# Kernel tuning notes

Measured on AMD Instinct MI355X. Metric: run time of the kernel, lower is better.

Reference implementation:

```python
import jax, jax.numpy as jnp
import numpy as np

B, LQ, LK, D, H, DK = 128, 32, 128, 1024, 16, 64


def setup_inputs() -> dict:
    key = jax.random.key(0)
    ks = jax.random.split(key, 10)
    Q_seq = jax.random.normal(ks[0], (B, LQ, D), dtype=jnp.float32)
    K_seq = jax.random.normal(ks[1], (B, LK, D), dtype=jnp.float32)
    V_seq = jax.random.normal(ks[2], (B, LK, D), dtype=jnp.float32)
    title_mask = (jax.random.uniform(ks[3], (B, LQ)) < 0.9).astype(jnp.float32)
    body_mask = (jax.random.uniform(ks[4], (B, LQ, LK)) < 0.9).astype(jnp.float32)
    s = 1.0 / np.sqrt(D)
    Wq = jax.random.uniform(ks[5], (H * DK, D), jnp.float32, -s, s)
    Wk = jax.random.uniform(ks[6], (H * DK, D), jnp.float32, -s, s)
    Wv = jax.random.uniform(ks[7], (H * DK, D), jnp.float32, -s, s)
    bq = jnp.zeros((H * DK,), jnp.float32)
    bk = jnp.zeros((H * DK,), jnp.float32)
    bv = jnp.zeros((H * DK,), jnp.float32)
    return {"Q_seq": Q_seq, "K_seq": K_seq, "V_seq": V_seq,
            "title_mask": title_mask, "body_mask": body_mask,
            "Wq": Wq, "bq": bq, "Wk": Wk, "bk": bk, "Wv": Wv, "bv": bv}


def reference(Q_seq, K_seq, V_seq, title_mask, body_mask, Wq, bq, Wk, bk, Wv, bv):
    b = Q_seq.shape[0]
    # concatenate title tokens onto keys/values: [B, LK+LQ, D]
    K_cat = jnp.concatenate([K_seq, Q_seq], axis=1)
    V_cat = jnp.concatenate([V_seq, Q_seq], axis=1)
    # mask: [B, LQ, LK+LQ]
    tmask_rep = jnp.broadcast_to(title_mask[:, None, :], (b, LQ, LQ))
    mask = jnp.concatenate([body_mask, tmask_rep], axis=2) * title_mask[:, :, None]
    # projections -> [B, H, len, DK]
    Qh = (Q_seq @ Wq.T + bq).reshape(b, LQ, H, DK).transpose(0, 2, 1, 3)
    Kh = (K_cat @ Wk.T + bk).reshape(b, LK + LQ, H, DK).transpose(0, 2, 1, 3)
    Vh = (V_cat @ Wv.T + bv).reshape(b, LK + LQ, H, DK).transpose(0, 2, 1, 3)
    # custom exp-based masked attention (non-softmax normalization)
    scores = jnp.einsum('bhqd,bhkd->bhqk', Qh, Kh) / np.sqrt(float(DK))
    scores = jnp.exp(scores) * mask[:, None, :, :]
    attn = scores / (jnp.sum(scores, axis=-1, keepdims=True) + 1e-8)
    ctx = jnp.einsum('bhqk,bhkd->bhqd', attn, Vh)
    return ctx.transpose(0, 2, 1, 3).reshape(b, LQ, H * DK)
```

## Files before the change

### kernel.cpp

```cpp
#include <hip/hip_runtime.h>

typedef _Float16 f16;
typedef _Float16 f16x4 __attribute__((ext_vector_type(4)));
typedef _Float16 f16x8 __attribute__((ext_vector_type(8)));
typedef float f32x4v __attribute__((ext_vector_type(4)));

#define AS1 __attribute__((address_space(1)))
#define AS3 __attribute__((address_space(3)))

__device__ __forceinline__ void gload_lds16(const f16* g, f16* l) {
  __builtin_amdgcn_global_load_lds((const AS1 unsigned int*)g,
                                   (AS3 unsigned int*)l, 16, 0, 0);
}

__global__ __launch_bounds__(256) void prep_kernel(
    const float* __restrict__ Q_seq, const float* __restrict__ K_seq,
    const float* __restrict__ V_seq,
    const float* __restrict__ Wq, const float* __restrict__ Wk,
    const float* __restrict__ Wv,
    f16* __restrict__ Qb, f16* __restrict__ Kb, f16* __restrict__ Vb,
    f16* __restrict__ Wqb, f16* __restrict__ Wkb, f16* __restrict__ Wvb)
{
  for (long long g = (long long)blockIdx.x * 256 + threadIdx.x;
       g < 5111808; g += (long long)2048 * 256) {
    const float* s;
    f16* d;
    if (g < 524288) {
      s = Q_seq + g * 8; d = Qb + g * 8;
    } else if (g < 2621440) {
      long long e = (g - 524288) * 8; s = K_seq + e; d = Kb + e;
    } else if (g < 4718592) {
      long long e = (g - 2621440) * 8; s = V_seq + e; d = Vb + e;
    } else if (g < 4849664) {
      long long e = (g - 4718592) * 8; s = Wq + e; d = Wqb + e;
    } else if (g < 4980736) {
      long long e = (g - 4849664) * 8; s = Wk + e; d = Wkb + e;
    } else {
      long long e = (g - 4980736) * 8; s = Wv + e; d = Wvb + e;
    }
    float4 v0 = *(const float4*)s;
    float4 v1 = *(const float4*)(s + 4);
    f16x8 o;
    o[0] = (f16)v0.x; o[1] = (f16)v0.y; o[2] = (f16)v0.z; o[3] = (f16)v0.w;
    o[4] = (f16)v1.x; o[5] = (f16)v1.y; o[6] = (f16)v1.z; o[7] = (f16)v1.w;
    *(f16x8*)d = o;
  }
}

__device__ __forceinline__ void gemm_tile_128(
    const f16* __restrict__ A, const f16* __restrict__ W,
    const float* __restrict__ bias, f16* __restrict__ C,
    int m0, int n0, int rowShift, int outStride, int rowOff,
    f16* sbuf)
{
  const int t = threadIdx.x;
  const int w = t >> 6, lane = t & 63;
  const int wr = w >> 1, wc = w & 1;
  const int fr = lane & 15, g = lane >> 4;
  const int kgr = (t & 7) ^ ((t >> 3) & 7);

  const f16* aS = A + (long long)(m0 + (t >> 3)) * 1024 + kgr * 8;
  const f16* bS = W + (long long)(n0 + (t >> 3)) * 1024 + kgr * 8;
  f16* lA = sbuf + w * 512;
  f16* lB = sbuf + 8192 + w * 512;

  const int gk0 = ((0 + g) ^ (fr & 7)) * 8;
  const int gk1 = ((4 + g) ^ (fr & 7)) * 8;
  const int aoff = (wr * 64 + fr) * 64;
  const int boff = (wc * 64 + fr) * 64;

  f32x4v acc[4][4];
#pragma unroll
  for (int i = 0; i < 4; ++i)
#pragma unroll
    for (int j = 0; j < 4; ++j) acc[i][j] = (f32x4v){0.f, 0.f, 0.f, 0.f};

  for (int tt = 0; tt < 16; ++tt) {
    const int ko = tt * 64;
#pragma unroll
    for (int s = 0; s < 4; ++s)
      gload_lds16(aS + s * 32768 + ko, lA + s * 2048);
#pragma unroll
    for (int s = 0; s < 4; ++s)
      gload_lds16(bS + s * 32768 + ko, lB + s * 2048);
    __syncthreads();

    f16x8 af[4], bf[4];
#pragma unroll
    for (int i = 0; i < 4; ++i)
      af[i] = *(const f16x8*)(sbuf + aoff + i * 1024 + gk0);
#pragma unroll
    for (int j = 0; j < 4; ++j)
      bf[j] = *(const f16x8*)(sbuf + 8192 + boff + j * 1024 + gk0);
#pragma unroll
    for (int i = 0; i < 4; ++i)
#pragma unroll
      for (int j = 0; j < 4; ++j)
        acc[i][j] = __builtin_amdgcn_mfma_f32_16x16x32_f16(af[i], bf[j],
                                                           acc[i][j], 0, 0, 0);
#pragma unroll
    for (int i = 0; i < 4; ++i)
      af[i] = *(const f16x8*)(sbuf + aoff + i * 1024 + gk1);
#pragma unroll
    for (int j = 0; j < 4; ++j)
      bf[j] = *(const f16x8*)(sbuf + 8192 + boff + j * 1024 + gk1);
#pragma unroll
    for (int i = 0; i < 4; ++i)
#pragma unroll
      for (int j = 0; j < 4; ++j)
        acc[i][j] = __builtin_amdgcn_mfma_f32_16x16x32_f16(af[i], bf[j],
                                                           acc[i][j], 0, 0, 0);

    __syncthreads();
  }

  f16* Cs = sbuf;
  float bn[4];
#pragma unroll
  for (int j = 0; j < 4; ++j) bn[j] = bias[n0 + wc * 64 + j * 16 + fr];
#pragma unroll
  for (int i = 0; i < 4; ++i) {
#pragma unroll
    for (int j = 0; j < 4; ++j) {
#pragma unroll
      for (int v = 0; v < 4; ++v) {
        int row = wr * 64 + i * 16 + g * 4 + v;
        int col = wc * 64 + j * 16 + fr;
        Cs[row * 136 + (col ^ ((row & 12) << 2))] = (f16)(acc[i][j][v] + bn[j]);
      }
    }
  }
  __syncthreads();

  const int rowMask = (1 << rowShift) - 1;
  const int row = t >> 1, half = t & 1;
  const int rsw = (row & 12) << 2;
  const int arow = m0 + row;
  const int orow = (arow >> rowShift) * outStride + (arow & rowMask) + rowOff;
  f16* dst = C + (long long)orow * 1024 + n0 + half * 64;
  const f16* srcr = Cs + row * 136;
#pragma unroll
  for (int c = 0; c < 8; ++c)
    *(f16x8*)(dst + c * 8) = *(const f16x8*)(srcr + ((half * 64 + c * 8) ^ rsw));
}

__global__ __launch_bounds__(256) void gemm_all(
    const f16* __restrict__ Qb, const f16* __restrict__ Kb,
    const f16* __restrict__ Vb,
    const f16* __restrict__ Wqb, const f16* __restrict__ Wkb,
    const f16* __restrict__ Wvb,
    const float* __restrict__ bq, const float* __restrict__ bk,
    const float* __restrict__ bv,
    f16* __restrict__ Qh, f16* __restrict__ Kh, f16* __restrict__ Vh)
{
  __shared__ __align__(16) f16 sbuf[17408];
  const int bid = blockIdx.x;
  const int v = (bid & 7) * 352 + (bid >> 3);

  const f16* A;
  const f16* W;
  const float* bias;
  f16* C;
  int m0, n0, rowShift, outStride, rowOff;

  if (v < 2048) {
    const int z = v >> 10, rem = v & 1023;
    A = z ? Vb : Kb;
    W = z ? Wvb : Wkb;
    bias = z ? bv : bk;
    C = z ? Vh : Kh;
    m0 = (rem >> 3) * 128; n0 = (rem & 7) * 128;
    rowShift = 7; outStride = 160; rowOff = 0;
  } else {
    const int u = v - 2048;
    const int z = u >> 8, rem = u & 255;
    A = Qb;
    W = (z == 0) ? Wqb : (z == 1) ? Wkb : Wvb;
    bias = (z == 0) ? bq : (z == 1) ? bk : bv;
    C = (z == 0) ? Qh : (z == 1) ? Kh : Vh;
    m0 = (rem >> 3) * 128; n0 = (rem & 7) * 128;
    rowShift = 5;
    outStride = (z == 0) ? 32 : 160;
    rowOff = (z == 0) ? 0 : 128;
  }
  gemm_tile_128(A, W, bias, C, m0, n0, rowShift, outStride, rowOff, sbuf);
}

__global__ __launch_bounds__(256) void attn_kernel(
    const f16* __restrict__ Qh, const f16* __restrict__ Kh,
    const f16* __restrict__ Vh,
    const float* __restrict__ title, const float* __restrict__ body,
    float* __restrict__ out)
{
  __shared__ __align__(16) f16 Qs[32 * 72];
  __shared__ __align__(16) f16 Ks[160 * 72];
  __shared__ __align__(16) f16 Vs[160 * 68];
  __shared__ float rs[4][32];
  __shared__ float invs[32];

  const int bh = blockIdx.x, b = bh >> 4, h = bh & 15;
  const int t = threadIdx.x, w = t >> 6, lane = t & 63;
  const int c = lane & 15, g = lane >> 4;

  const long long qbase = ((long long)(b * 32) << 10) + h * 64;
  const long long kbase = ((long long)(b * 160) << 10) + h * 64;

  {
    int row = t >> 3, ch = t & 7;
    *(f16x8*)(Qs + row * 72 + ch * 8) =
        *(const f16x8*)(Qh + qbase + (long long)row * 1024 + ch * 8);
  }
#pragma unroll
  for (int r = 0; r < 5; ++r) {
    int i = t + r * 256;
    int row = i >> 3, ch = i & 7;
    *(f16x8*)(Ks + row * 72 + ch * 8) =
        *(const f16x8*)(Kh + kbase + (long long)row * 1024 + ch * 8);
    f16x8 vv = *(const f16x8*)(Vh + kbase + (long long)row * 1024 + ch * 8);
    f16x4 vlo = __builtin_shufflevector(vv, vv, 0, 1, 2, 3);
    f16x4 vhi = __builtin_shufflevector(vv, vv, 4, 5, 6, 7);
    *(f16x4*)(Vs + row * 68 + ch * 8) = vlo;
    *(f16x4*)(Vs + row * 68 + ch * 8 + 4) = vhi;
  }
  __syncthreads();

  f16x8 qf[2][2];
#pragma unroll
  for (int qt = 0; qt < 2; ++qt)
#pragma unroll
    for (int s = 0; s < 2; ++s)
      qf[qt][s] = *(const f16x8*)(Qs + (qt * 16 + c) * 72 + s * 32 + g * 8);

  const int cnt = (w < 2) ? 3 : 2;
  const int tile0 = (w < 2) ? w * 3 : 6 + (w - 2) * 2;

  f16x4 pp[3][2];
  float rsum[2] = {0.f, 0.f};

#pragma unroll
  for (int i = 0; i < 3; ++i) {
    if (i < cnt) {
      const int kt = tile0 + i;
      f16x8 kf0 = *(const f16x8*)(Ks + (kt * 16 + c) * 72 + 0 + g * 8);
      f16x8 kf1 = *(const f16x8*)(Ks + (kt * 16 + c) * 72 + 32 + g * 8);
#pragma unroll
      for (int qt = 0; qt < 2; ++qt) {
        f32x4v s4 = (f32x4v){0.f, 0.f, 0.f, 0.f};
        s4 = __builtin_amdgcn_mfma_f32_16x16x32_f16(kf0, qf[qt][0], s4, 0, 0, 0);
        s4 = __builtin_amdgcn_mfma_f32_16x16x32_f16(kf1, qf[qt][1], s4, 0, 0, 0);
        float4 m4;
        if (kt < 8) {
          m4 = *(const float4*)(body +
                ((long long)(b * 32 + qt * 16 + c)) * 128 + kt * 16 + 4 * g);
        } else {
          m4 = *(const float4*)(title + b * 32 + (kt - 8) * 16 + 4 * g);
        }
        float e0 = __expf(s4[0] * 0.125f) * m4.x;
        float e1 = __expf(s4[1] * 0.125f) * m4.y;
        float e2 = __expf(s4[2] * 0.125f) * m4.z;
        float e3 = __expf(s4[3] * 0.125f) * m4.w;
        rsum[qt] += (e0 + e1) + (e2 + e3);
        f16x4 p4;
        p4.x = (f16)e0; p4.y = (f16)e1; p4.z = (f16)e2; p4.w = (f16)e3;
        pp[i][qt] = p4;
      }
    }
  }

#pragma unroll
  for (int qt = 0; qt < 2; ++qt) {
    rsum[qt] += __shfl_xor(rsum[qt], 16);
    rsum[qt] += __shfl_xor(rsum[qt], 32);
  }
  if (lane < 16) {
    rs[w][c] = rsum[0];
    rs[w][16 + c] = rsum[1];
  }
  __syncthreads();

  f16* Ps = Ks;
#pragma unroll
  for (int i = 0; i < 3; ++i) {
    if (i < cnt) {
      const int kt = tile0 + i;
#pragma unroll
      for (int qt = 0; qt < 2; ++qt)
        *(f16x4*)(Ps + (qt * 16 + c) * 168 + kt * 16 + 4 * g) = pp[i][qt];
    }
  }
  if (t < 32) {
    float ssum = rs[0][t] + rs[1][t] + rs[2][t] + rs[3][t];
    invs[t] = title[b * 32 + t] / (ssum + 1e-8f);
  }
  __syncthreads();

  f32x4v o[2] = {(f32x4v){0.f, 0.f, 0.f, 0.f}, (f32x4v){0.f, 0.f, 0.f, 0.f}};
#pragma unroll
  for (int s = 0; s < 5; ++s) {
    f16x8 vf;
#pragma unroll
    for (int j = 0; j < 8; ++j)
      vf[j] = Vs[(32 * s + 8 * g + j) * 68 + 16 * w + c];
#pragma unroll
    for (int qt = 0; qt < 2; ++qt) {
      f16x8 pf = *(const f16x8*)(Ps + (qt * 16 + c) * 168 + s * 32 + g * 8);
      o[qt] = __builtin_amdgcn_mfma_f32_16x16x32_f16(pf, vf, o[qt], 0, 0, 0);
    }
  }

#pragma unroll
  for (int qt = 0; qt < 2; ++qt) {
#pragma unroll
    for (int v = 0; v < 4; ++v) {
      int q = qt * 16 + 4 * g + v;
      out[((long long)(b * 32 + q) << 10) + h * 64 + 16 * w + c] =
          o[qt][v] * invs[q];
    }
  }
}

extern "C" void kernel_launch(void* const* d_in, const int* in_sizes, int n_in,
                              void* d_out, int out_size, void* d_ws, size_t ws_size,
                              hipStream_t stream) {
  const float* Q_seq = (const float*)d_in[0];
  const float* K_seq = (const float*)d_in[1];
  const float* V_seq = (const float*)d_in[2];
  const float* title = (const float*)d_in[3];
  const float* body  = (const float*)d_in[4];
  const float* Wq = (const float*)d_in[5];
  const float* bq = (const float*)d_in[6];
  const float* Wk = (const float*)d_in[7];
  const float* bk = (const float*)d_in[8];
  const float* Wv = (const float*)d_in[9];
  const float* bv = (const float*)d_in[10];
  float* out = (float*)d_out;

  f16* ws = (f16*)d_ws;
  f16* Qb  = ws;
  f16* Kb  = Qb + 4194304;
  f16* Vb  = Kb + 16777216;
  f16* Wqb = Vb + 16777216;
  f16* Wkb = Wqb + 1048576;
  f16* Wvb = Wkb + 1048576;
  f16* Qh  = Wvb + 1048576;
  f16* Kh  = Qh + 4194304;
  f16* Vh  = Kh + 20971520;

  prep_kernel<<<2048, 256, 0, stream>>>(Q_seq, K_seq, V_seq, Wq, Wk, Wv,
                                        Qb, Kb, Vb, Wqb, Wkb, Wvb);
  gemm_all<<<2816, 256, 0, stream>>>(Qb, Kb, Vb, Wqb, Wkb, Wvb,
                                     bq, bk, bv, Qh, Kh, Vh);
  attn_kernel<<<2048, 256, 0, stream>>>(Qh, Kh, Vh, title, body, out);
}
```

Before: 192.3 us.

## Fuse fp32-to-fp16 activation conversion into GEMM tile loads

Result: faster. 174.4 us (-9.3%).

```diff
diff --git a/kernel.cpp b/kernel.cpp
--- a/kernel.cpp
+++ b/kernel.cpp
@@ -13,42 +13,31 @@
                                    (AS3 unsigned int*)l, 16, 0, 0);
 }
 
-__global__ __launch_bounds__(256) void prep_kernel(
-    const float* __restrict__ Q_seq, const float* __restrict__ K_seq,
-    const float* __restrict__ V_seq,
+__global__ __launch_bounds__(256) void prep_w(
     const float* __restrict__ Wq, const float* __restrict__ Wk,
     const float* __restrict__ Wv,
-    f16* __restrict__ Qb, f16* __restrict__ Kb, f16* __restrict__ Vb,
     f16* __restrict__ Wqb, f16* __restrict__ Wkb, f16* __restrict__ Wvb)
 {
-  for (long long g = (long long)blockIdx.x * 256 + threadIdx.x;
-       g < 5111808; g += (long long)2048 * 256) {
-    const float* s;
-    f16* d;
-    if (g < 524288) {
-      s = Q_seq + g * 8; d = Qb + g * 8;
-    } else if (g < 2621440) {
-      long long e = (g - 524288) * 8; s = K_seq + e; d = Kb + e;
-    } else if (g < 4718592) {
-      long long e = (g - 2621440) * 8; s = V_seq + e; d = Vb + e;
-    } else if (g < 4849664) {
-      long long e = (g - 4718592) * 8; s = Wq + e; d = Wqb + e;
-    } else if (g < 4980736) {
-      long long e = (g - 4849664) * 8; s = Wk + e; d = Wkb + e;
-    } else {
-      long long e = (g - 4980736) * 8; s = Wv + e; d = Wvb + e;
-    }
-    float4 v0 = *(const float4*)s;
-    float4 v1 = *(const float4*)(s + 4);
-    f16x8 o;
-    o[0] = (f16)v0.x; o[1] = (f16)v0.y; o[2] = (f16)v0.z; o[3] = (f16)v0.w;
-    o[4] = (f16)v1.x; o[5] = (f16)v1.y; o[6] = (f16)v1.z; o[7] = (f16)v1.w;
-    *(f16x8*)d = o;
-  }
-}
-
-__device__ __forceinline__ void gemm_tile_128(
-    const f16* __restrict__ A, const f16* __restrict__ W,
+  const long long g = (long long)blockIdx.x * 256 + threadIdx.x;
+  const float* s;
+  f16* d;
+  if (g < 131072) {
+    s = Wq + g * 8; d = Wqb + g * 8;
+  } else if (g < 262144) {
+    long long e = (g - 131072) * 8; s = Wk + e; d = Wkb + e;
+  } else {
+    long long e = (g - 262144) * 8; s = Wv + e; d = Wvb + e;
+  }
+  float4 v0 = *(const float4*)s;
+  float4 v1 = *(const float4*)(s + 4);
+  f16x8 o;
+  o[0] = (f16)v0.x; o[1] = (f16)v0.y; o[2] = (f16)v0.z; o[3] = (f16)v0.w;
+  o[4] = (f16)v1.x; o[5] = (f16)v1.y; o[6] = (f16)v1.z; o[7] = (f16)v1.w;
+  *(f16x8*)d = o;
+}
+
+__device__ __forceinline__ void gemm_tile_128_f32A(
+    const float* __restrict__ A, const f16* __restrict__ W,
     const float* __restrict__ bias, f16* __restrict__ C,
     int m0, int n0, int rowShift, int outStride, int rowOff,
     f16* sbuf)
@@ -57,41 +46,63 @@
   const int w = t >> 6, lane = t & 63;
   const int wr = w >> 1, wc = w & 1;
   const int fr = lane & 15, g = lane >> 4;
-  const int kgr = (t & 7) ^ ((t >> 3) & 7);
-
-  const f16* aS = A + (long long)(m0 + (t >> 3)) * 1024 + kgr * 8;
-  const f16* bS = W + (long long)(n0 + (t >> 3)) * 1024 + kgr * 8;
-  f16* lA = sbuf + w * 512;
-  f16* lB = sbuf + 8192 + w * 512;
-
-  const int gk0 = ((0 + g) ^ (fr & 7)) * 8;
-  const int gk1 = ((4 + g) ^ (fr & 7)) * 8;
+
+  const int arow4 = lane >> 4;
+  const int ax = w * 4 + arow4;
+  const float* aSrc = A + (long long)(m0 + ax) * 1024 + ((lane & 15) ^ ax) * 4;
+
+  const int brow = lane >> 3;
+  const f16* bSrc = W + (long long)(n0 + w * 8 + brow) * 1024 +
+                    ((lane & 7) ^ brow) * 8;
+
+  const float* Asl = (const float*)sbuf;
+  const f16* Bsl = sbuf + 16384;
+
   const int aoff = (wr * 64 + fr) * 64;
   const int boff = (wc * 64 + fr) * 64;
+  const int gkB0 = ((0 + g) ^ (fr & 7)) * 8;
+  const int gkB1 = ((4 + g) ^ (fr & 7)) * 8;
+  const int pa0 = ((2 * g) ^ fr) * 4;
+  const int pa1 = ((2 * (4 + g)) ^ fr) * 4;
 
   f32x4v acc[4][4];
 #pragma unroll
   for (int i = 0; i < 4; ++i)
 #pragma unroll
     for (int j = 0; j < 4; ++j) acc[i][j] = (f32x4v){0.f, 0.f, 0.f, 0.f};
+
+#define CVT8(dst, p)                                                         \
+  {                                                                          \
+    float4 q0_ = *(const float4*)(p);                                        \
+    float4 q1_ = *(const float4*)((p) + ((pa_sw) ? -4 : 4));                 \
+    dst[0] = (f16)q0_.x; dst[1] = (f16)q0_.y;                                \
+    dst[2] = (f16)q0_.z; dst[3] = (f16)q0_.w;                                \
+    dst[4] = (f16)q1_.x; dst[5] = (f16)q1_.y;                                \
+    dst[6] = (f16)q1_.z; dst[7] = (f16)q1_.w;                                \
+  }
+  const bool pa_sw = (fr & 1);
 
   for (int tt = 0; tt < 16; ++tt) {
     const int ko = tt * 64;
 #pragma unroll
+    for (int s = 0; s < 8; ++s)
+      gload_lds16((const f16*)(aSrc + (long long)s * 16 * 1024 + ko),
+                  sbuf + (s * 4 + w) * 512);
+#pragma unroll
     for (int s = 0; s < 4; ++s)
-      gload_lds16(aS + s * 32768 + ko, lA + s * 2048);
-#pragma unroll
-    for (int s = 0; s < 4; ++s)
-      gload_lds16(bS + s * 32768 + ko, lB + s * 2048);
+      gload_lds16(bSrc + (long long)s * 32 * 1024 + ko,
+                  sbuf + 16384 + (s * 4 + w) * 512);
     __syncthreads();
 
     f16x8 af[4], bf[4];
 #pragma unroll
-    for (int i = 0; i < 4; ++i)
-      af[i] = *(const f16x8*)(sbuf + aoff + i * 1024 + gk0);
+    for (int i = 0; i < 4; ++i) {
+      const float* p = Asl + aoff + i * 1024 + pa0;
+      CVT8(af[i], p);
+    }
 #pragma unroll
     for (int j = 0; j < 4; ++j)
-      bf[j] = *(const f16x8*)(sbuf + 8192 + boff + j * 1024 + gk0);
+      bf[j] = *(const f16x8*)(Bsl + boff + j * 1024 + gkB0);
 #pragma unroll
     for (int i = 0; i < 4; ++i)
 #pragma unroll
@@ -99,11 +110,13 @@
         acc[i][j] = __builtin_amdgcn_mfma_f32_16x16x32_f16(af[i], bf[j],
                                                            acc[i][j], 0, 0, 0);
 #pragma unroll
-    for (int i = 0; i < 4; ++i)
-      af[i] = *(const f16x8*)(sbuf + aoff + i * 1024 + gk1);
+    for (int i = 0; i < 4; ++i) {
+      const float* p = Asl + aoff + i * 1024 + pa1;
+      CVT8(af[i], p);
+    }
 #pragma unroll
     for (int j = 0; j < 4; ++j)
-      bf[j] = *(const f16x8*)(sbuf + 8192 + boff + j * 1024 + gk1);
+      bf[j] = *(const f16x8*)(Bsl + boff + j * 1024 + gkB1);
 #pragma unroll
     for (int i = 0; i < 4; ++i)
 #pragma unroll
@@ -113,6 +126,8 @@
 
     __syncthreads();
   }
+#undef CVT8
+
 
   f16* Cs = sbuf;
   float bn[4];
@@ -145,19 +160,19 @@
 }
 
 __global__ __launch_bounds__(256) void gemm_all(
-    const f16* __restrict__ Qb, const f16* __restrict__ Kb,
-    const f16* __restrict__ Vb,
+    const float* __restrict__ Q_seq, const float* __restrict__ K_seq,
+    const float* __restrict__ V_seq,
     const f16* __restrict__ Wqb, const f16* __restrict__ Wkb,
     const f16* __restrict__ Wvb,
     const float* __restrict__ bq, const float* __restrict__ bk,
     const float* __restrict__ bv,
     f16* __restrict__ Qh, f16* __restrict__ Kh, f16* __restrict__ Vh)
 {
-  __shared__ __align__(16) f16 sbuf[17408];
+  __shared__ __align__(16) f16 sbuf[24576];
   const int bid = blockIdx.x;
   const int v = (bid & 7) * 352 + (bid >> 3);
 
-  const f16* A;
+  const float* A;
   const f16* W;
   const float* bias;
   f16* C;
@@ -165,7 +180,7 @@
 
   if (v < 2048) {
     const int z = v >> 10, rem = v & 1023;
-    A = z ? Vb : Kb;
+    A = z ? V_seq : K_seq;
     W = z ? Wvb : Wkb;
     bias = z ? bv : bk;
     C = z ? Vh : Kh;
@@ -174,7 +189,7 @@
   } else {
     const int u = v - 2048;
     const int z = u >> 8, rem = u & 255;
-    A = Qb;
+    A = Q_seq;
     W = (z == 0) ? Wqb : (z == 1) ? Wkb : Wvb;
     bias = (z == 0) ? bq : (z == 1) ? bk : bv;
     C = (z == 0) ? Qh : (z == 1) ? Kh : Vh;
@@ -183,7 +198,7 @@
     outStride = (z == 0) ? 32 : 160;
     rowOff = (z == 0) ? 0 : 128;
   }
-  gemm_tile_128(A, W, bias, C, m0, n0, rowShift, outStride, rowOff, sbuf);
+  gemm_tile_128_f32A(A, W, bias, C, m0, n0, rowShift, outStride, rowOff, sbuf);
 }
 
 __global__ __launch_bounds__(256) void attn_kernel(
@@ -336,19 +351,15 @@
   float* out = (float*)d_out;
 
   f16* ws = (f16*)d_ws;
-  f16* Qb  = ws;
-  f16* Kb  = Qb + 4194304;
-  f16* Vb  = Kb + 16777216;
-  f16* Wqb = Vb + 16777216;
+  f16* Wqb = ws;
   f16* Wkb = Wqb + 1048576;
   f16* Wvb = Wkb + 1048576;
   f16* Qh  = Wvb + 1048576;
   f16* Kh  = Qh + 4194304;
   f16* Vh  = Kh + 20971520;
 
-  prep_kernel<<<2048, 256, 0, stream>>>(Q_seq, K_seq, V_seq, Wq, Wk, Wv,
-                                        Qb, Kb, Vb, Wqb, Wkb, Wvb);
-  gemm_all<<<2816, 256, 0, stream>>>(Qb, Kb, Vb, Wqb, Wkb, Wvb,
+  prep_w<<<1536, 256, 0, stream>>>(Wq, Wk, Wv, Wqb, Wkb, Wvb);
+  gemm_all<<<2816, 256, 0, stream>>>(Q_seq, K_seq, V_seq, Wqb, Wkb, Wvb,
                                      bq, bk, bv, Qh, Kh, Vh);
   attn_kernel<<<2048, 256, 0, stream>>>(Qh, Kh, Vh, title, body, out);
 }
```
